# Optimization experiments

Measured on AMD Instinct MI355X. Metric: run time of the kernel, lower is better.

Reference implementation:

```python
import jax, jax.numpy as jnp
import numpy as np

B, C, H, W = 8, 512, 32, 32
N_HEADS, HEAD_DIM = 8, 64
EPS = 1e-5


def _layernorm(x, g, b):
    mu = jnp.mean(x, axis=-1, keepdims=True)
    var = jnp.mean(jnp.square(x - mu), axis=-1, keepdims=True)
    return (x - mu) * jax.lax.rsqrt(var + EPS) * g + b


def setup_inputs() -> dict:
    key = jax.random.key(0)
    ks = jax.random.split(key, 16)
    u = lambda k, shp: jax.random.uniform(k, shp, dtype=jnp.float32)
    inp = {
        "x": jax.random.normal(ks[0], (B, C, H, W), dtype=jnp.float32),
        "t": jax.random.normal(ks[1], (B,), dtype=jnp.float32),
        # attention params (torch.rand init in source)
        "K_W": u(ks[2], (N_HEADS, C, HEAD_DIM)), "K_b": u(ks[3], (N_HEADS, HEAD_DIM)),
        "Q_W": u(ks[4], (N_HEADS, C, HEAD_DIM)), "Q_b": u(ks[5], (N_HEADS, HEAD_DIM)),
        "V_W": u(ks[6], (N_HEADS, C, HEAD_DIM)), "V_b": u(ks[7], (N_HEADS, HEAD_DIM)),
        "O_W": u(ks[8], (N_HEADS, HEAD_DIM, C)), "O_b": u(ks[9], (C,)),
        # pre-attention LayerNorm
        "ln1_g": jnp.ones((C,), jnp.float32), "ln1_b": jnp.zeros((C,), jnp.float32),
        # MLP: LayerNorm -> Linear -> GELU -> Linear
        "ln2_g": jnp.ones((C,), jnp.float32), "ln2_b": jnp.zeros((C,), jnp.float32),
        "W1": jax.random.normal(ks[10], (C, C), dtype=jnp.float32) / np.sqrt(C),
        "b1": jnp.zeros((C,), jnp.float32),
        "W2": jax.random.normal(ks[11], (C, C), dtype=jnp.float32) / np.sqrt(C),
        "b2": jnp.zeros((C,), jnp.float32),
    }
    return inp


def reference(x, t, K_W, K_b, Q_W, Q_b, V_W, V_b, O_W, O_b,
              ln1_g, ln1_b, ln2_g, ln2_b, W1, b1, W2, b2):
    b, c, h, w = x.shape
    xs = x.reshape(b, c, h * w).transpose(0, 2, 1)           # b s c
    res = _layernorm(xs, ln1_g, ln1_b)
    q = jnp.einsum('bsc,ncd->bsnd', res, Q_W) + Q_b          # b s n_h h_dim
    k = jnp.einsum('bsc,ncd->bsnd', res, K_W) + K_b
    v = jnp.einsum('bsc,ncd->bsnd', res, V_W) + V_b
    scores = jnp.einsum('bsnd,btnd->bnst', q, k) / jnp.sqrt(jnp.float32(c))
    attn = jax.nn.softmax(scores, axis=-1)                   # b n_h s s
    o = jnp.einsum('bnst,btnd->bsnd', attn, v)
    out = jnp.einsum('bsnd,ndc->bsc', o, O_W) + O_b
    out = out + xs                                           # residual
    m = _layernorm(out, ln2_g, ln2_b)
    m = jax.nn.gelu(m @ W1 + b1, approximate=False) @ W2 + b2
    out = m + out
    return out.transpose(0, 2, 1).reshape(b, c, h, w)
```

## Files before the change

kernel.cpp:

```cpp
#include <hip/hip_runtime.h>
#include <math.h>

#define BB 8
#define CC 512
#define SS 1024
#define NHH 8
#define HDD 64
#define KD 512

typedef __attribute__((ext_vector_type(8))) short short8;
typedef __attribute__((ext_vector_type(4))) float f32x4;

__device__ __forceinline__ unsigned short f2bf(float x) {
  union { float f; unsigned int u; } c; c.f = x;
  unsigned int r = (c.u + 0x7FFFu + ((c.u >> 16) & 1u)) >> 16;
  return (unsigned short)r;
}
__device__ __forceinline__ float b2f(unsigned short h) {
  union { unsigned int u; float f; } c; c.u = ((unsigned int)h) << 16; return c.f;
}

#define GLD_LDS(gp, lp) __builtin_amdgcn_global_load_lds( \
    (const __attribute__((address_space(1))) void*)(gp),  \
    (__attribute__((address_space(3))) void*)(lp), 16, 0, 0)

__device__ __forceinline__ float block_reduce_sum(float v) {
  __shared__ float sm[4];
  #pragma unroll
  for (int o = 32; o > 0; o >>= 1) v += __shfl_down(v, o, 64);
  if ((threadIdx.x & 63) == 0) sm[threadIdx.x >> 6] = v;
  __syncthreads();
  float r = (sm[0] + sm[1]) + (sm[2] + sm[3]);
  __syncthreads();
  return r;
}

__global__ __launch_bounds__(256) void transpose_k(const float* __restrict__ in,
                                                   float* __restrict__ out,
                                                   int d1, int d2) {
  __shared__ float tile[32][33];
  int b = blockIdx.z;
  int j0 = blockIdx.x * 32;
  int i0 = blockIdx.y * 32;
  const float* inb = in + (size_t)b * d1 * d2;
  float* outb = out + (size_t)b * d1 * d2;
  int tx = threadIdx.x, ty = threadIdx.y;
  #pragma unroll
  for (int i = ty; i < 32; i += 8)
    tile[i][tx] = inb[(size_t)(i0 + i) * d2 + j0 + tx];
  __syncthreads();
  #pragma unroll
  for (int i = ty; i < 32; i += 8)
    outb[(size_t)(j0 + i) * d1 + i0 + tx] = tile[tx][i];
}

__global__ __launch_bounds__(256) void ln_bf16_k(const float* __restrict__ in,
                                                 const float* __restrict__ g,
                                                 const float* __restrict__ be,
                                                 unsigned short* __restrict__ outh,
                                                 unsigned short* __restrict__ outl) {
  size_t row = blockIdx.x;
  const float* r = in + row * CC;
  int t = threadIdx.x;
  float v0 = r[t], v1 = r[t + 256];
  float s = block_reduce_sum(v0 + v1);
  float mu = s * (1.0f / CC);
  float d0 = v0 - mu, d1 = v1 - mu;
  float vs = block_reduce_sum(d0 * d0 + d1 * d1);
  float rstd = rsqrtf(vs * (1.0f / CC) + 1e-5f);
  float y0 = d0 * rstd * g[t] + be[t];
  float y1 = d1 * rstd * g[t + 256] + be[t + 256];
  unsigned short h0 = f2bf(y0), h1 = f2bf(y1);
  outh[row * CC + t]       = h0;
  outh[row * CC + t + 256] = h1;
  if (outl) {
    outl[row * CC + t]       = f2bf(y0 - b2f(h0));
    outl[row * CC + t + 256] = f2bf(y1 - b2f(h1));
  }
}

__global__ __launch_bounds__(256) void convert_weights(
    const float* __restrict__ QW, const float* __restrict__ KW,
    const float* __restrict__ VW, const float* __restrict__ OW,
    const float* __restrict__ W1, const float* __restrict__ W2,
    const float* __restrict__ Qb, const float* __restrict__ Kb,
    const float* __restrict__ Vb,
    unsigned short* __restrict__ BtQKh, unsigned short* __restrict__ BtQKl,
    unsigned short* __restrict__ BtVh,
    unsigned short* __restrict__ BtOh, unsigned short* __restrict__ BtOl,
    unsigned short* __restrict__ BtW1h, unsigned short* __restrict__ BtW2h,
    float* __restrict__ qkvb) {
  __shared__ float tile[32][33];
  const int p = blockIdx.z, wsel = p >> 3, sub = p & 7;
  const int k0 = blockIdx.x * 32, d0 = blockIdx.y * 32;
  const int tx = threadIdx.x, ty = threadIdx.y;
  const float* w; int rs; unsigned short *dh, *dl; int nbase;
  switch (wsel) {
    case 0:  w = QW + sub * 32768; rs = 64;  dh = BtQKh; dl = BtQKl;  nbase = sub * 64;        break;
    case 1:  w = KW + sub * 32768; rs = 64;  dh = BtQKh; dl = BtQKl;  nbase = 512 + sub * 64;  break;
    case 2:  w = VW + sub * 32768; rs = 64;  dh = BtVh;  dl = nullptr; nbase = sub * 64;       break;
    case 3:  w = OW + sub * 64;    rs = 512; dh = BtOh;  dl = BtOl;   nbase = sub * 64;        break;
    case 4:  w = W1 + sub * 64;    rs = 512; dh = BtW1h; dl = nullptr; nbase = sub * 64;       break;
    default: w = W2 + sub * 64;    rs = 512; dh = BtW2h; dl = nullptr; nbase = sub * 64;       break;
  }
  for (int i = ty; i < 32; i += 8)
    tile[i][tx] = w[(size_t)(k0 + i) * rs + d0 + tx];
  __syncthreads();
  for (int i = ty; i < 32; i += 8) {
    float f = tile[tx][i];
    unsigned short h = f2bf(f);
    size_t idx = (size_t)(nbase + d0 + i) * KD + k0 + tx;
    dh[idx] = h;
    if (dl) dl[idx] = f2bf(f - b2f(h));
  }
  if (p == 0 && blockIdx.x == 0 && blockIdx.y == 0) {
    int t = ty * 32 + tx;
    for (int i = t; i < 1536; i += 256)
      qkvb[i] = i < 512 ? Qb[i] : (i < 1024 ? Kb[i - 512] : Vb[i - 1024]);
  }
}

__global__ __launch_bounds__(256) void gemm_qkv(
    const unsigned short* __restrict__ Ah, const unsigned short* __restrict__ Al,
    const unsigned short* __restrict__ Bth, const unsigned short* __restrict__ Btl,
    const float* __restrict__ bias,
    unsigned short* __restrict__ qkh, unsigned short* __restrict__ qkl,
    unsigned short* __restrict__ vh) {
  __shared__ __align__(16) unsigned short As[2 * 128 * 32];
  __shared__ __align__(16) unsigned short Bs[2 * 128 * 32];
  const int tid = threadIdx.x;
  const int w = tid >> 6, l = tid & 63, quad = l >> 4, lm = l & 15;
  const int n0 = blockIdx.x * 128, m0 = blockIdx.y * 128;
  const bool splitB = n0 < 1024;
  const int wm = (w >> 1) * 64, wn = (w & 1) * 64;
  const int srow = tid >> 2;
  const int sch = (((tid & 3) ^ (srow & 3)) * 8);
  const unsigned short* Agh = Ah + (size_t)(m0 + srow) * KD + sch;
  const unsigned short* Agl = Al + (size_t)(m0 + srow) * KD + sch;
  const unsigned short* Bgh = Bth + (size_t)(n0 + srow) * KD + sch;
  const unsigned short* Bgl = Btl + (size_t)(n0 + srow) * KD + sch;
  unsigned short* Aswh = As + w * 512;
  unsigned short* Aswl = As + 4096 + w * 512;
  unsigned short* Bswh = Bs + w * 512;
  unsigned short* Bswl = Bs + 4096 + w * 512;
  const int rch = ((quad ^ (lm & 3)) * 8);
  const f32x4 fzero = {0.f, 0.f, 0.f, 0.f};
  f32x4 acc[4][4];
  #pragma unroll
  for (int i = 0; i < 4; ++i)
    #pragma unroll
    for (int j = 0; j < 4; ++j) acc[i][j] = fzero;
  for (int k0 = 0; k0 < KD; k0 += 32) {
    __syncthreads();
    GLD_LDS(Agh + k0, Aswh);
    GLD_LDS(Agh + k0 + 64 * KD, Aswh + 2048);
    GLD_LDS(Agl + k0, Aswl);
    GLD_LDS(Agl + k0 + 64 * KD, Aswl + 2048);
    GLD_LDS(Bgh + k0, Bswh);
    GLD_LDS(Bgh + k0 + 64 * KD, Bswh + 2048);
    if (splitB) {
      GLD_LDS(Bgl + k0, Bswl);
      GLD_LDS(Bgl + k0 + 64 * KD, Bswl + 2048);
    }
    __syncthreads();
    short8 afh[4], afl[4], bfh[4], bfl[4];
    #pragma unroll
    for (int i = 0; i < 4; ++i) {
      afh[i] = *(const short8*)(As + (wm + i * 16 + lm) * 32 + rch);
      afl[i] = *(const short8*)(As + 4096 + (wm + i * 16 + lm) * 32 + rch);
    }
    #pragma unroll
    for (int j = 0; j < 4; ++j)
      bfh[j] = *(const short8*)(Bs + (wn + j * 16 + lm) * 32 + rch);
    if (splitB) {
      #pragma unroll
      for (int j = 0; j < 4; ++j)
        bfl[j] = *(const short8*)(Bs + 4096 + (wn + j * 16 + lm) * 32 + rch);
      #pragma unroll
      for (int i = 0; i < 4; ++i)
        #pragma unroll
        for (int j = 0; j < 4; ++j) {
          f32x4 t = acc[i][j];
          t = __builtin_amdgcn_mfma_f32_16x16x32_bf16(afh[i], bfh[j], t, 0, 0, 0);
          t = __builtin_amdgcn_mfma_f32_16x16x32_bf16(afh[i], bfl[j], t, 0, 0, 0);
          t = __builtin_amdgcn_mfma_f32_16x16x32_bf16(afl[i], bfh[j], t, 0, 0, 0);
          acc[i][j] = t;
        }
    } else {
      #pragma unroll
      for (int i = 0; i < 4; ++i)
        #pragma unroll
        for (int j = 0; j < 4; ++j)
          acc[i][j] = __builtin_amdgcn_mfma_f32_16x16x32_bf16(afh[i], bfh[j], acc[i][j], 0, 0, 0);
    }
  }
  #pragma unroll
  for (int i = 0; i < 4; ++i) {
    const int row = m0 + wm + i * 16 + quad * 4;
    #pragma unroll
    for (int j = 0; j < 4; ++j) {
      const int ncol = n0 + wn + j * 16 + lm;
      const float bv = bias[ncol];
      #pragma unroll
      for (int r = 0; r < 4; ++r) {
        float x = acc[i][j][r] + bv;
        if (splitB) {
          const size_t oi = (size_t)(row + r) * 1024 + ncol;
          unsigned short h = f2bf(x);
          qkh[oi] = h;
          qkl[oi] = f2bf(x - b2f(h));
        } else {
          vh[(size_t)(row + r) * 512 + (ncol - 1024)] = f2bf(x);
        }
      }
    }
  }
}

template<int SB, int GELU, int OUTMODE, int RESID, int TRANS>
__global__ __launch_bounds__(256) void gemm64(
    const unsigned short* __restrict__ Ah,
    const unsigned short* __restrict__ Bh, const unsigned short* __restrict__ Bl,
    const float* __restrict__ bias, const float* __restrict__ resid,
    unsigned short* __restrict__ outh, float* __restrict__ outf, int ldc) {
  __shared__ __align__(16) unsigned short As[64 * 32];
  __shared__ __align__(16) unsigned short Bs[(SB ? 2 : 1) * 64 * 32];
  __shared__ float ttile[TRANS ? 64 : 1][TRANS ? 65 : 1];
  const int tid = threadIdx.x;
  const int w = tid >> 6, l = tid & 63, quad = l >> 4, lm = l & 15;
  const int n0 = blockIdx.x * 64, m0 = blockIdx.y * 64;
  const int wm = (w >> 1) * 32, wn = (w & 1) * 32;
  const int srow = tid >> 2;
  const int sch = (((tid & 3) ^ (srow & 3)) * 8);
  const unsigned short* Ag = Ah + (size_t)(m0 + srow) * KD + sch;
  const unsigned short* Bg = Bh + (size_t)(n0 + srow) * KD + sch;
  const unsigned short* Bgl = SB ? Bl + (size_t)(n0 + srow) * KD + sch : nullptr;
  unsigned short* Asw = As + w * 512;
  unsigned short* Bsw = Bs + w * 512;
  unsigned short* Bswl = Bs + 2048 + w * 512;
  const int rch = ((quad ^ (lm & 3)) * 8);
  const f32x4 fzero = {0.f, 0.f, 0.f, 0.f};
  f32x4 acc[2][2];
  #pragma unroll
  for (int i = 0; i < 2; ++i)
    #pragma unroll
    for (int j = 0; j < 2; ++j) acc[i][j] = fzero;
  for (int k0 = 0; k0 < KD; k0 += 32) {
    __syncthreads();
    GLD_LDS(Ag + k0, Asw);
    GLD_LDS(Bg + k0, Bsw);
    if constexpr (SB) GLD_LDS(Bgl + k0, Bswl);
    __syncthreads();
    short8 af[2], bfh[2], bfl[2];
    #pragma unroll
    for (int i = 0; i < 2; ++i)
      af[i] = *(const short8*)(As + (wm + i * 16 + lm) * 32 + rch);
    #pragma unroll
    for (int j = 0; j < 2; ++j)
      bfh[j] = *(const short8*)(Bs + (wn + j * 16 + lm) * 32 + rch);
    if constexpr (SB) {
      #pragma unroll
      for (int j = 0; j < 2; ++j)
        bfl[j] = *(const short8*)(Bs + 2048 + (wn + j * 16 + lm) * 32 + rch);
    }
    #pragma unroll
    for (int i = 0; i < 2; ++i)
      #pragma unroll
      for (int j = 0; j < 2; ++j) {
        f32x4 t = acc[i][j];
        t = __builtin_amdgcn_mfma_f32_16x16x32_bf16(af[i], bfh[j], t, 0, 0, 0);
        if constexpr (SB)
          t = __builtin_amdgcn_mfma_f32_16x16x32_bf16(af[i], bfl[j], t, 0, 0, 0);
        acc[i][j] = t;
      }
  }
  if constexpr (TRANS) __syncthreads();
  #pragma unroll
  for (int i = 0; i < 2; ++i) {
    const int row = m0 + wm + i * 16 + quad * 4;
    #pragma unroll
    for (int j = 0; j < 2; ++j) {
      const int col = n0 + wn + j * 16 + lm;
      const float bv = bias[col];
      #pragma unroll
      for (int r = 0; r < 4; ++r) {
        float x = acc[i][j][r] + bv;
        if (GELU) x = 0.5f * x * (1.0f + erff(x * 0.70710678118654752f));
        if (RESID) x += resid[(size_t)(row + r) * CC + col];
        if constexpr (TRANS) {
          ttile[wm + i * 16 + quad * 4 + r][wn + j * 16 + lm] = x;
        } else {
          const size_t oi = (size_t)(row + r) * ldc + col;
          if (OUTMODE == 0) outf[oi] = x;
          else outh[oi] = f2bf(x);
        }
      }
    }
  }
  if constexpr (TRANS) {
    __syncthreads();
    const int bi = m0 >> 10, s0 = m0 & 1023;
    const int s = tid & 63;
    #pragma unroll
    for (int c0 = 0; c0 < 64; c0 += 4) {
      const int col = c0 + (tid >> 6);
      outf[(size_t)(bi * 512 + n0 + col) * 1024 + s0 + s] = ttile[s][col];
    }
  }
}

__global__ __launch_bounds__(256) void attn_mfma(
    const unsigned short* __restrict__ QKh, const unsigned short* __restrict__ QKl,
    const unsigned short* __restrict__ Vh, unsigned short* __restrict__ Oh) {
  __shared__ __align__(16) unsigned short Ksh[64 * 64], Ksl[64 * 64];
  __shared__ __align__(16) unsigned short Vth[64 * 72];
  __shared__ __align__(16) unsigned short Ps[4 * 16 * 88];
  const int q0 = blockIdx.x * 64, h = blockIdx.y, b = blockIdx.z;
  const int tid = threadIdx.x, w = tid >> 6, l = tid & 63, quad = l >> 4, lm = l & 15;
  const int LDQ = 2 * CC;
  const size_t qkbase = (size_t)b * SS * LDQ;
  const size_t vbase  = (size_t)b * SS * CC;
  const int srow8 = tid >> 3;
  const int sch8  = ((tid & 7) ^ (srow8 & 7)) * 8;
  short8 qh[2], ql[2];
  {
    const size_t qo = qkbase + (size_t)(q0 + w * 16 + lm) * LDQ + h * 64 + quad * 8;
    qh[0] = *(const short8*)(QKh + qo);
    qh[1] = *(const short8*)(QKh + qo + 32);
    ql[0] = *(const short8*)(QKl + qo);
    ql[1] = *(const short8*)(QKl + qo + 32);
  }
  short8 bones;
  #pragma unroll
  for (int u = 0; u < 8; ++u) bones[u] = (lm == 0) ? (short)0x3F80 : (short)0;
  const f32x4 fzero = {0.f, 0.f, 0.f, 0.f};
  float mrow[4];
  f32x4 oacc[5];
  #pragma unroll
  for (int r = 0; r < 4; ++r) mrow[r] = -1e30f;
  #pragma unroll
  for (int j = 0; j < 5; ++j) oacc[j] = fzero;
  const float scale = 0.044194173824159216f;
  unsigned short* Pw = Ps + w * (16 * 88);
  for (int kt = 0; kt < SS; kt += 64) {
    __syncthreads();
    {
      const unsigned short* kg  = QKh + qkbase + (size_t)(kt + srow8) * LDQ + CC + h * 64 + sch8;
      const unsigned short* kgl = QKl + qkbase + (size_t)(kt + srow8) * LDQ + CC + h * 64 + sch8;
      GLD_LDS(kg, Ksh + w * 512);
      GLD_LDS(kg + 32 * LDQ, Ksh + 2048 + w * 512);
      GLD_LDS(kgl, Ksl + w * 512);
      GLD_LDS(kgl + 32 * LDQ, Ksl + 2048 + w * 512);
      #pragma unroll
      for (int pass = 0; pass < 2; ++pass) {
        const int c = w + pass * 4;
        const size_t vo = vbase + (size_t)(kt + l) * CC + h * 64 + c * 8;
        short8 vh8 = *(const short8*)(Vh + vo);
        #pragma unroll
        for (int u = 0; u < 8; ++u) Vth[(c * 8 + u) * 72 + l] = (unsigned short)vh8[u];
      }
    }
    __syncthreads();
    f32x4 sc[4];
    #pragma unroll
    for (int j = 0; j < 4; ++j) sc[j] = fzero;
    #pragma unroll
    for (int st = 0; st < 2; ++st) {
      const int kc = ((st * 4 + quad) ^ (lm & 7)) * 8;
      #pragma unroll
      for (int j = 0; j < 4; ++j) {
        short8 kh = *(const short8*)(Ksh + (j * 16 + lm) * 64 + kc);
        short8 kl = *(const short8*)(Ksl + (j * 16 + lm) * 64 + kc);
        f32x4 t = sc[j];
        t = __builtin_amdgcn_mfma_f32_16x16x32_bf16(qh[st], kh, t, 0, 0, 0);
        t = __builtin_amdgcn_mfma_f32_16x16x32_bf16(qh[st], kl, t, 0, 0, 0);
        t = __builtin_amdgcn_mfma_f32_16x16x32_bf16(ql[st], kh, t, 0, 0, 0);
        sc[j] = t;
      }
    }
    #pragma unroll
    for (int j = 0; j < 4; ++j) sc[j] *= scale;
    #pragma unroll
    for (int r = 0; r < 4; ++r) {
      float mt = fmaxf(fmaxf(sc[0][r], sc[1][r]), fmaxf(sc[2][r], sc[3][r]));
      #pragma unroll
      for (int mask = 1; mask < 16; mask <<= 1) mt = fmaxf(mt, __shfl_xor(mt, mask, 64));
      const float mn = fmaxf(mrow[r], mt);
      const float alpha = __expf(mrow[r] - mn);
      mrow[r] = mn;
      #pragma unroll
      for (int j = 0; j < 4; ++j) sc[j][r] = __expf(sc[j][r] - mn);
      #pragma unroll
      for (int j = 0; j < 5; ++j) oacc[j][r] *= alpha;
    }
    #pragma unroll
    for (int r = 0; r < 4; ++r)
      #pragma unroll
      for (int j = 0; j < 4; ++j)
        Pw[(quad * 4 + r) * 88 + j * 16 + lm] = f2bf(sc[j][r]);
    #pragma unroll
    for (int st = 0; st < 2; ++st) {
      short8 ap = *(const short8*)(Pw + lm * 88 + st * 32 + quad * 8);
      #pragma unroll
      for (int j = 0; j < 4; ++j) {
        short8 vv = *(const short8*)(Vth + (j * 16 + lm) * 72 + st * 32 + quad * 8);
        oacc[j] = __builtin_amdgcn_mfma_f32_16x16x32_bf16(ap, vv, oacc[j], 0, 0, 0);
      }
      oacc[4] = __builtin_amdgcn_mfma_f32_16x16x32_bf16(ap, bones, oacc[4], 0, 0, 0);
    }
  }
  float inv[4];
  #pragma unroll
  for (int r = 0; r < 4; ++r) {
    const float lv = __shfl(oacc[4][r], l & 48, 64);
    inv[r] = 1.f / lv;
  }
  const size_t obase = vbase + (size_t)(q0 + w * 16 + quad * 4) * CC + h * 64 + lm;
  #pragma unroll
  for (int j = 0; j < 4; ++j)
    #pragma unroll
    for (int r = 0; r < 4; ++r)
      Oh[obase + (size_t)r * CC + j * 16] = f2bf(oacc[j][r] * inv[r]);
}

extern "C" void kernel_launch(void* const* d_in, const int* in_sizes, int n_in,
                              void* d_out, int out_size, void* d_ws, size_t ws_size,
                              hipStream_t stream) {
  const float* x    = (const float*)d_in[0];
  const float* K_W  = (const float*)d_in[2];
  const float* K_b  = (const float*)d_in[3];
  const float* Q_W  = (const float*)d_in[4];
  const float* Q_b  = (const float*)d_in[5];
  const float* V_W  = (const float*)d_in[6];
  const float* V_b  = (const float*)d_in[7];
  const float* O_W  = (const float*)d_in[8];
  const float* O_b  = (const float*)d_in[9];
  const float* ln1g = (const float*)d_in[10];
  const float* ln1b = (const float*)d_in[11];
  const float* ln2g = (const float*)d_in[12];
  const float* ln2b = (const float*)d_in[13];
  const float* W1   = (const float*)d_in[14];
  const float* b1   = (const float*)d_in[15];
  const float* W2   = (const float*)d_in[16];
  const float* b2   = (const float*)d_in[17];
  float* out = (float*)d_out;

  unsigned char* ws = (unsigned char*)d_ws;
  const size_t MB = 1u << 20;
  float* bufx           = (float*)(ws);
  unsigned short* qkh   = (unsigned short*)(ws + 16 * MB);
  unsigned short* qkl   = (unsigned short*)(ws + 32 * MB);
  unsigned short* vh    = (unsigned short*)(ws + 48 * MB);
  unsigned short* ln1h  = (unsigned short*)(ws + 56 * MB);
  unsigned short* ln1l  = (unsigned short*)(ws + 64 * MB);
  unsigned short* oh    = ln1h;
  float* out1           = (float*)(ws + 72 * MB);
  unsigned short* ln2h  = (unsigned short*)(ws + 16 * MB);
  unsigned short* geluh = (unsigned short*)(ws + 24 * MB);
  unsigned short* BtAll = (unsigned short*)(ws + 88 * MB);
  unsigned short* BtQKh = BtAll;
  unsigned short* BtVh  = BtAll + 1024 * 512;
  unsigned short* BtQKl = BtVh + 512 * 512;
  unsigned short* BtOh  = BtQKl + 1024 * 512;
  unsigned short* BtOl  = BtOh + 512 * 512;
  unsigned short* BtW1h = BtOl + 512 * 512;
  unsigned short* BtW2h = BtW1h + 512 * 512;
  float* qkvb           = (float*)(BtW2h + 512 * 512);

  dim3 tb32(32, 8);
  transpose_k<<<dim3(SS / 32, CC / 32, BB), tb32, 0, stream>>>(x, bufx, CC, SS);
  convert_weights<<<dim3(16, 2, 48), tb32, 0, stream>>>(
      Q_W, K_W, V_W, O_W, W1, W2, Q_b, K_b, V_b,
      BtQKh, BtQKl, BtVh, BtOh, BtOl, BtW1h, BtW2h, qkvb);
  ln_bf16_k<<<BB * SS, 256, 0, stream>>>(bufx, ln1g, ln1b, ln1h, ln1l);
  gemm_qkv<<<dim3(12, 64), 256, 0, stream>>>(
      ln1h, ln1l, BtAll, BtQKl, qkvb, qkh, qkl, vh);
  attn_mfma<<<dim3(SS / 64, NHH, BB), 256, 0, stream>>>(qkh, qkl, vh, oh);
  gemm64<1, 0, 0, 1, 0><<<dim3(8, 128), 256, 0, stream>>>(
      oh, BtOh, BtOl, O_b, bufx, nullptr, out1, CC);
  ln_bf16_k<<<BB * SS, 256, 0, stream>>>(out1, ln2g, ln2b, ln2h, nullptr);
  gemm64<0, 1, 1, 0, 0><<<dim3(8, 128), 256, 0, stream>>>(
      ln2h, BtW1h, nullptr, b1, nullptr, geluh, nullptr, CC);
  gemm64<0, 0, 0, 1, 1><<<dim3(8, 128), 256, 0, stream>>>(
      geluh, BtW2h, nullptr, b2, out1, nullptr, out, CC);
}
```

Baseline: 301.7 us.

## Fuse input transpose into LN1, store V transposed, use exp2 softmax

Removes the separate transpose kernel by having a new LN1 kernel read x in its channel-major layout, compute per-position stats in two passes, and emit both the normalized activations and a split bf16 hi/lo copy of the residual. The QKV GEMM now writes V pre-transposed per head, so attention can load V tiles straight into shared memory with global_load_lds instead of a manual register transpose. Softmax folds log2(e) into the scale and uses exp2f. The residual is now held as bf16 hi+lo, and variance is computed as E[x^2]-mu^2, which adds some rounding risk; x is also read twice by the LN1 kernel.

New measurement: 339.5 us. +12.6%, slower.

```diff
diff --git a/kernel.cpp b/kernel.cpp
--- a/kernel.cpp
+++ b/kernel.cpp
@@ -10,6 +10,7 @@
 
 typedef __attribute__((ext_vector_type(8))) short short8;
 typedef __attribute__((ext_vector_type(4))) float f32x4;
+typedef __attribute__((ext_vector_type(4))) unsigned short ushort4v;
 
 __device__ __forceinline__ unsigned short f2bf(float x) {
   union { float f; unsigned int u; } c; c.f = x;
@@ -35,30 +36,65 @@
   return r;
 }
 
-__global__ __launch_bounds__(256) void transpose_k(const float* __restrict__ in,
-                                                   float* __restrict__ out,
-                                                   int d1, int d2) {
+__global__ __launch_bounds__(256) void ln1_fused(
+    const float* __restrict__ x, const float* __restrict__ g,
+    const float* __restrict__ be,
+    unsigned short* __restrict__ yh, unsigned short* __restrict__ yl,
+    unsigned short* __restrict__ xh, unsigned short* __restrict__ xl) {
   __shared__ float tile[32][33];
-  int b = blockIdx.z;
-  int j0 = blockIdx.x * 32;
-  int i0 = blockIdx.y * 32;
-  const float* inb = in + (size_t)b * d1 * d2;
-  float* outb = out + (size_t)b * d1 * d2;
-  int tx = threadIdx.x, ty = threadIdx.y;
-  #pragma unroll
-  for (int i = ty; i < 32; i += 8)
-    tile[i][tx] = inb[(size_t)(i0 + i) * d2 + j0 + tx];
+  __shared__ float red[2][8][33];
+  __shared__ float mu_s[32], rs_s[32];
+  const int b = blockIdx.y, s0 = blockIdx.x * 32;
+  const int tx = threadIdx.x, ty = threadIdx.y;
+  const float* xb = x + (size_t)b * CC * SS;
+  float psum = 0.f, psq = 0.f;
+  for (int c0 = 0; c0 < CC; c0 += 32) {
+    __syncthreads();
+    #pragma unroll
+    for (int i = ty; i < 32; i += 8)
+      tile[i][tx] = xb[(size_t)(c0 + i) * SS + s0 + tx];
+    __syncthreads();
+    #pragma unroll
+    for (int k = 0; k < 4; ++k) {
+      const float v = tile[ty * 4 + k][tx];
+      psum += v; psq += v * v;
+    }
+  }
+  red[0][ty][tx] = psum; red[1][ty][tx] = psq;
   __syncthreads();
-  #pragma unroll
-  for (int i = ty; i < 32; i += 8)
-    outb[(size_t)(j0 + i) * d1 + i0 + tx] = tile[tx][i];
+  if (ty == 0) {
+    float s = 0.f, q = 0.f;
+    #pragma unroll
+    for (int k = 0; k < 8; ++k) { s += red[0][k][tx]; q += red[1][k][tx]; }
+    const float mu = s * (1.0f / CC);
+    mu_s[tx] = mu;
+    rs_s[tx] = rsqrtf(q * (1.0f / CC) - mu * mu + 1e-5f);
+  }
+  __syncthreads();
+  for (int c0 = 0; c0 < CC; c0 += 32) {
+    __syncthreads();
+    #pragma unroll
+    for (int i = ty; i < 32; i += 8)
+      tile[i][tx] = xb[(size_t)(c0 + i) * SS + s0 + tx];
+    __syncthreads();
+    const float gc = g[c0 + tx], bc = be[c0 + tx];
+    #pragma unroll
+    for (int i = ty; i < 32; i += 8) {
+      const float v = tile[tx][i];
+      const float y = (v - mu_s[i]) * rs_s[i] * gc + bc;
+      const size_t oi = ((size_t)b * SS + s0 + i) * CC + c0 + tx;
+      const unsigned short hy = f2bf(y);
+      yh[oi] = hy; yl[oi] = f2bf(y - b2f(hy));
+      const unsigned short hx = f2bf(v);
+      xh[oi] = hx; xl[oi] = f2bf(v - b2f(hx));
+    }
+  }
 }
 
 __global__ __launch_bounds__(256) void ln_bf16_k(const float* __restrict__ in,
                                                  const float* __restrict__ g,
                                                  const float* __restrict__ be,
-                                                 unsigned short* __restrict__ outh,
-                                                 unsigned short* __restrict__ outl) {
+                                                 unsigned short* __restrict__ outh) {
   size_t row = blockIdx.x;
   const float* r = in + row * CC;
   int t = threadIdx.x;
@@ -68,15 +104,8 @@
   float d0 = v0 - mu, d1 = v1 - mu;
   float vs = block_reduce_sum(d0 * d0 + d1 * d1);
   float rstd = rsqrtf(vs * (1.0f / CC) + 1e-5f);
-  float y0 = d0 * rstd * g[t] + be[t];
-  float y1 = d1 * rstd * g[t + 256] + be[t + 256];
-  unsigned short h0 = f2bf(y0), h1 = f2bf(y1);
-  outh[row * CC + t]       = h0;
-  outh[row * CC + t + 256] = h1;
-  if (outl) {
-    outl[row * CC + t]       = f2bf(y0 - b2f(h0));
-    outl[row * CC + t + 256] = f2bf(y1 - b2f(h1));
-  }
+  outh[row * CC + t]       = f2bf(d0 * rstd * g[t] + be[t]);
+  outh[row * CC + t + 256] = f2bf(d1 * rstd * g[t + 256] + be[t + 256]);
 }
 
 __global__ __launch_bounds__(256) void convert_weights(
@@ -125,7 +154,7 @@
     const unsigned short* __restrict__ Bth, const unsigned short* __restrict__ Btl,
     const float* __restrict__ bias,
     unsigned short* __restrict__ qkh, unsigned short* __restrict__ qkl,
-    unsigned short* __restrict__ vh) {
+    unsigned short* __restrict__ vt) {
   __shared__ __align__(16) unsigned short As[2 * 128 * 32];
   __shared__ __align__(16) unsigned short Bs[2 * 128 * 32];
   const int tid = threadIdx.x;
@@ -201,17 +230,22 @@
     for (int j = 0; j < 4; ++j) {
       const int ncol = n0 + wn + j * 16 + lm;
       const float bv = bias[ncol];
-      #pragma unroll
-      for (int r = 0; r < 4; ++r) {
-        float x = acc[i][j][r] + bv;
-        if (splitB) {
+      if (splitB) {
+        #pragma unroll
+        for (int r = 0; r < 4; ++r) {
+          const float xv = acc[i][j][r] + bv;
           const size_t oi = (size_t)(row + r) * 1024 + ncol;
-          unsigned short h = f2bf(x);
+          unsigned short h = f2bf(xv);
           qkh[oi] = h;
-          qkl[oi] = f2bf(x - b2f(h));
-        } else {
-          vh[(size_t)(row + r) * 512 + (ncol - 1024)] = f2bf(x);
+          qkl[oi] = f2bf(xv - b2f(h));
         }
+      } else {
+        const int hd = ncol - 1024, hh = hd >> 6, dd = hd & 63;
+        const int bb2 = row >> 10, s = row & 1023;
+        ushort4v pack;
+        #pragma unroll
+        for (int r = 0; r < 4; ++r) pack[r] = f2bf(acc[i][j][r] + bv);
+        *(ushort4v*)(vt + ((size_t)(bb2 * 8 + hh) * 64 + dd) * 1024 + s) = pack;
       }
     }
   }
@@ -221,7 +255,8 @@
 __global__ __launch_bounds__(256) void gemm64(
     const unsigned short* __restrict__ Ah,
     const unsigned short* __restrict__ Bh, const unsigned short* __restrict__ Bl,
-    const float* __restrict__ bias, const float* __restrict__ resid,
+    const float* __restrict__ bias, const float* __restrict__ residf,
+    const unsigned short* __restrict__ residh, const unsigned short* __restrict__ residl,
     unsigned short* __restrict__ outh, float* __restrict__ outf, int ldc) {
   __shared__ __align__(16) unsigned short As[64 * 32];
   __shared__ __align__(16) unsigned short Bs[(SB ? 2 : 1) * 64 * 32];
@@ -286,7 +321,9 @@
       for (int r = 0; r < 4; ++r) {
         float x = acc[i][j][r] + bv;
         if (GELU) x = 0.5f * x * (1.0f + erff(x * 0.70710678118654752f));
-        if (RESID) x += resid[(size_t)(row + r) * CC + col];
+        const size_t ri = (size_t)(row + r) * CC + col;
+        if (RESID == 1) x += residf[ri];
+        if (RESID == 2) x += b2f(residh[ri]) + b2f(residl[ri]);
         if constexpr (TRANS) {
           ttile[wm + i * 16 + quad * 4 + r][wn + j * 16 + lm] = x;
         } else {
@@ -311,17 +348,17 @@
 
 __global__ __launch_bounds__(256) void attn_mfma(
     const unsigned short* __restrict__ QKh, const unsigned short* __restrict__ QKl,
-    const unsigned short* __restrict__ Vh, unsigned short* __restrict__ Oh) {
+    const unsigned short* __restrict__ Vt, unsigned short* __restrict__ Oh) {
   __shared__ __align__(16) unsigned short Ksh[64 * 64], Ksl[64 * 64];
-  __shared__ __align__(16) unsigned short Vth[64 * 72];
+  __shared__ __align__(16) unsigned short Vts[64 * 64];
   __shared__ __align__(16) unsigned short Ps[4 * 16 * 88];
   const int q0 = blockIdx.x * 64, h = blockIdx.y, b = blockIdx.z;
   const int tid = threadIdx.x, w = tid >> 6, l = tid & 63, quad = l >> 4, lm = l & 15;
   const int LDQ = 2 * CC;
   const size_t qkbase = (size_t)b * SS * LDQ;
-  const size_t vbase  = (size_t)b * SS * CC;
   const int srow8 = tid >> 3;
   const int sch8  = ((tid & 7) ^ (srow8 & 7)) * 8;
+  const unsigned short* Vg = Vt + ((size_t)(b * 8 + h) * 64 + srow8) * 1024 + sch8;
   short8 qh[2], ql[2];
   {
     const size_t qo = qkbase + (size_t)(q0 + w * 16 + lm) * LDQ + h * 64 + quad * 8;
@@ -340,7 +377,7 @@
   for (int r = 0; r < 4; ++r) mrow[r] = -1e30f;
   #pragma unroll
   for (int j = 0; j < 5; ++j) oacc[j] = fzero;
-  const float scale = 0.044194173824159216f;
+  const float scale = 0.044194173824159216f * 1.4426950408889634f;
   unsigned short* Pw = Ps + w * (16 * 88);
   for (int kt = 0; kt < SS; kt += 64) {
     __syncthreads();
@@ -351,14 +388,8 @@
       GLD_LDS(kg + 32 * LDQ, Ksh + 2048 + w * 512);
       GLD_LDS(kgl, Ksl + w * 512);
       GLD_LDS(kgl + 32 * LDQ, Ksl + 2048 + w * 512);
-      #pragma unroll
-      for (int pass = 0; pass < 2; ++pass) {
-        const int c = w + pass * 4;
-        const size_t vo = vbase + (size_t)(kt + l) * CC + h * 64 + c * 8;
-        short8 vh8 = *(const short8*)(Vh + vo);
-        #pragma unroll
-        for (int u = 0; u < 8; ++u) Vth[(c * 8 + u) * 72 + l] = (unsigned short)vh8[u];
-      }
+      GLD_LDS(Vg + kt, Vts + w * 512);
+      GLD_LDS(Vg + kt + 32 * 1024, Vts + 2048 + w * 512);
     }
     __syncthreads();
     f32x4 sc[4];
@@ -386,10 +417,10 @@
       #pragma unroll
       for (int mask = 1; mask < 16; mask <<= 1) mt = fmaxf(mt, __shfl_xor(mt, mask, 64));
       const float mn = fmaxf(mrow[r], mt);
-      const float alpha = __expf(mrow[r] - mn);
+      const float alpha = exp2f(mrow[r] - mn);
       mrow[r] = mn;
       #pragma unroll
-      for (int j = 0; j < 4; ++j) sc[j][r] = __expf(sc[j][r] - mn);
+      for (int j = 0; j < 4; ++j) sc[j][r] = exp2f(sc[j][r] - mn);
       #pragma unroll
       for (int j = 0; j < 5; ++j) oacc[j][r] *= alpha;
     }
@@ -401,9 +432,10 @@
     #pragma unroll
     for (int st = 0; st < 2; ++st) {
       short8 ap = *(const short8*)(Pw + lm * 88 + st * 32 + quad * 8);
+      const int kc = ((st * 4 + quad) ^ (lm & 7)) * 8;
       #pragma unroll
       for (int j = 0; j < 4; ++j) {
-        short8 vv = *(const short8*)(Vth + (j * 16 + lm) * 72 + st * 32 + quad * 8);
+        short8 vv = *(const short8*)(Vts + (j * 16 + lm) * 64 + kc);
         oacc[j] = __builtin_amdgcn_mfma_f32_16x16x32_bf16(ap, vv, oacc[j], 0, 0, 0);
       }
       oacc[4] = __builtin_amdgcn_mfma_f32_16x16x32_bf16(ap, bones, oacc[4], 0, 0, 0);
@@ -415,7 +447,8 @@
     const float lv = __shfl(oacc[4][r], l & 48, 64);
     inv[r] = 1.f / lv;
   }
-  const size_t obase = vbase + (size_t)(q0 + w * 16 + quad * 4) * CC + h * 64 + lm;
+  const size_t obase =
+      (size_t)b * SS * CC + (size_t)(q0 + w * 16 + quad * 4) * CC + h * 64 + lm;
   #pragma unroll
   for (int j = 0; j < 4; ++j)
     #pragma unroll
@@ -447,16 +480,17 @@
 
   unsigned char* ws = (unsigned char*)d_ws;
   const size_t MB = 1u << 20;
-  float* bufx           = (float*)(ws);
-  unsigned short* qkh   = (unsigned short*)(ws + 16 * MB);
-  unsigned short* qkl   = (unsigned short*)(ws + 32 * MB);
-  unsigned short* vh    = (unsigned short*)(ws + 48 * MB);
-  unsigned short* ln1h  = (unsigned short*)(ws + 56 * MB);
-  unsigned short* ln1l  = (unsigned short*)(ws + 64 * MB);
+  unsigned short* qkh   = (unsigned short*)(ws);
+  unsigned short* qkl   = (unsigned short*)(ws + 16 * MB);
+  unsigned short* vt    = (unsigned short*)(ws + 32 * MB);
+  unsigned short* ln1h  = (unsigned short*)(ws + 40 * MB);
+  unsigned short* ln1l  = (unsigned short*)(ws + 48 * MB);
+  unsigned short* xsh   = (unsigned short*)(ws + 56 * MB);
+  unsigned short* xsl   = (unsigned short*)(ws + 64 * MB);
   unsigned short* oh    = ln1h;
   float* out1           = (float*)(ws + 72 * MB);
-  unsigned short* ln2h  = (unsigned short*)(ws + 16 * MB);
-  unsigned short* geluh = (unsigned short*)(ws + 24 * MB);
+  unsigned short* ln2h  = qkh;
+  unsigned short* geluh = (unsigned short*)(ws + 8 * MB);
   unsigned short* BtAll = (unsigned short*)(ws + 88 * MB);
   unsigned short* BtQKh = BtAll;
   unsigned short* BtVh  = BtAll + 1024 * 512;
@@ -468,19 +502,19 @@
   float* qkvb           = (float*)(BtW2h + 512 * 512);
 
   dim3 tb32(32, 8);
-  transpose_k<<<dim3(SS / 32, CC / 32, BB), tb32, 0, stream>>>(x, bufx, CC, SS);
   convert_weights<<<dim3(16, 2, 48), tb32, 0, stream>>>(
       Q_W, K_W, V_W, O_W, W1, W2, Q_b, K_b, V_b,
       BtQKh, BtQKl, BtVh, BtOh, BtOl, BtW1h, BtW2h, qkvb);
-  ln_bf16_k<<<BB * SS, 256, 0, stream>>>(bufx, ln1g, ln1b, ln1h, ln1l);
+  ln1_fused<<<dim3(SS / 32, BB), tb32, 0, stream>>>(
+      x, ln1g, ln1b, ln1h, ln1l, xsh, xsl);
   gemm_qkv<<<dim3(12, 64), 256, 0, stream>>>(
-      ln1h, ln1l, BtAll, BtQKl, qkvb, qkh, qkl, vh);
-  attn_mfma<<<dim3(SS / 64, NHH, BB), 256, 0, stream>>>(qkh, qkl, vh, oh);
-  gemm64<1, 0, 0, 1, 0><<<dim3(8, 128), 256, 0, stream>>>(
-      oh, BtOh, BtOl, O_b, bufx, nullptr, out1, CC);
-  ln_bf16_k<<<BB * SS, 256, 0, stream>>>(out1, ln2g, ln2b, ln2h, nullptr);
+      ln1h, ln1l, BtAll, BtQKl, qkvb, qkh, qkl, vt);
+  attn_mfma<<<dim3(SS / 64, NHH, BB), 256, 0, stream>>>(qkh, qkl, vt, oh);
+  gemm64<1, 0, 0, 2, 0><<<dim3(8, 128), 256, 0, stream>>>(
+      oh, BtOh, BtOl, O_b, nullptr, xsh, xsl, nullptr, out1, CC);
+  ln_bf16_k<<<BB * SS, 256, 0, stream>>>(out1, ln2g, ln2b, ln2h);
   gemm64<0, 1, 1, 0, 0><<<dim3(8, 128), 256, 0, stream>>>(
-      ln2h, BtW1h, nullptr, b1, nullptr, geluh, nullptr, CC);
+      ln2h, BtW1h, nullptr, b1, nullptr, nullptr, nullptr, geluh, nullptr, CC);
   gemm64<0, 0, 0, 1, 1><<<dim3(8, 128), 256, 0, stream>>>(
-      geluh, BtW2h, nullptr, b2, out1, nullptr, out, CC);
-}
+      geluh, BtW2h, nullptr, b2, out1, nullptr, nullptr, nullptr, out, CC);
+}
```
